# Performance work log

Measured on AMD Instinct MI355X. Metric: run time of the kernel, lower is better.

Reference implementation:

```python
import jax, jax.numpy as jnp
import numpy as np

MAX_DISP = 48


def setup_inputs() -> dict:
    key = jax.random.key(0)
    k1, k2 = jax.random.split(key)
    b, c, h, w = 2, 32, 96, 320
    left_feature = jax.random.normal(k1, (b, c, h, w), dtype=jnp.float32)
    right_feature = jax.random.normal(k2, (b, c, h, w), dtype=jnp.float32)
    return {"left_feature": left_feature, "right_feature": right_feature}


def reference(left_feature, right_feature):
    # volume[b, c, d, h, w] = left[b, c, h, w] - right[b, c, h, w - d]  if w >= d else 0
    b, c, h, w = left_feature.shape
    d_idx = jnp.arange(MAX_DISP)[:, None]          # [D, 1]
    w_idx = jnp.arange(w)[None, :]                 # [1, W]
    src = w_idx - d_idx                            # [D, W] source column in right feature
    valid = src >= 0                               # [D, W]
    src_c = jnp.clip(src, 0, w - 1)
    # gather shifted right feature: [b, c, h, D, W] -> [b, c, D, h, W]
    right_shift = right_feature[:, :, :, src_c].transpose(0, 1, 3, 2, 4)
    diff = left_feature[:, :, None, :, :] - right_shift
    volume = jnp.where(valid[None, None, :, None, :], diff, jnp.float32(0))
    return volume
```

## Files before the change

kernel.cpp:

```cpp
#include <hip/hip_runtime.h>

#define BB 2
#define CC 32
#define HH 96
#define WW 320
#define DD 48

__global__ __launch_bounds__(320) void diffvol_kernel(
        const float* __restrict__ left,
        const float* __restrict__ right,
        float* __restrict__ out) {
    __shared__ float rrow[WW];

    const int tid = threadIdx.x;
    const int blk = blockIdx.x;
    const int y   = blk % HH;
    const int bc  = blk / HH;

    const int base = (bc * HH + y) * WW;
    const float lv = left[base + tid];
    rrow[tid] = right[base + tid];
    __syncthreads();

    float* o = out + ((bc * DD) * HH + y) * WW + tid;
    const int dstride = HH * WW;

    if (tid >= 64) {
        #pragma unroll
        for (int d = 0; d < DD; ++d) {
            o[d * dstride] = lv - rrow[tid - d];
        }
    } else {
        #pragma unroll
        for (int d = 0; d < DD; ++d) {
            o[d * dstride] = (tid >= d) ? lv - rrow[tid - d] : 0.0f;
        }
    }
}

extern "C" void kernel_launch(void* const* d_in, const int* in_sizes, int n_in,
                              void* d_out, int out_size, void* d_ws, size_t ws_size,
                              hipStream_t stream) {
    const float* left  = (const float*)d_in[0];
    const float* right = (const float*)d_in[1];
    float* out = (float*)d_out;

    const int grid = BB * CC * HH;
    diffvol_kernel<<<grid, 320, 0, stream>>>(left, right, out);
}
```

Before: 388.8 us.

## Restructure grid to one block per (bc, disparity) with float4 stores and XCD-aware mapping

Each block now handles one (batch*channel, disparity) pair and walks all rows of the slice, writing contiguous float4 stores to a single output plane. Right-feature values are read directly from global memory with unaligned scalar loads, and the shared-memory staging is dropped. Block IDs are remapped so that blocks sharing a bc slice land on the same XCD for L2 reuse, and the starting row group is staggered by disparity to spread accesses. Because left and right slices are re-read once per disparity, the kernel depends on cache hits to avoid extra traffic.

```diff
diff --git a/kernel.cpp b/kernel.cpp
--- a/kernel.cpp
+++ b/kernel.cpp
@@ -5,36 +5,60 @@
 #define HH 96
 #define WW 320
 #define DD 48
+#define NBC   (BB * CC)
+#define SLICE (HH * WW)
+#define W4    (WW / 4)
+#define RPG   4
+#define NIT   (HH / RPG)
 
 __global__ __launch_bounds__(320) void diffvol_kernel(
         const float* __restrict__ left,
         const float* __restrict__ right,
         float* __restrict__ out) {
-    __shared__ float rrow[WW];
+    const int bid = blockIdx.x;
+    const int xcd = bid & 7;
+    const int loc = bid >> 3;
+    const int bc  = xcd * (NBC / 8) + loc / DD;
+    const int d   = loc % DD;
 
     const int tid = threadIdx.x;
-    const int blk = blockIdx.x;
-    const int y   = blk % HH;
-    const int bc  = blk / HH;
+    const int r   = tid / W4;
+    const int c   = tid % W4;
+    const int x0  = c * 4;
 
-    const int base = (bc * HH + y) * WW;
-    const float lv = left[base + tid];
-    rrow[tid] = right[base + tid];
-    __syncthreads();
+    const float* lslice = left  + bc * SLICE;
+    const float* rslice = right + bc * SLICE;
+    float*       oslice = out + (bc * DD + d) * SLICE;
 
-    float* o = out + ((bc * DD) * HH + y) * WW + tid;
-    const int dstride = HH * WW;
+    const int g0 = d % NIT;
+    const int sb = x0 - d;
 
-    if (tid >= 64) {
-        #pragma unroll
-        for (int d = 0; d < DD; ++d) {
-            o[d * dstride] = lv - rrow[tid - d];
+    for (int it = 0; it < NIT; ++it) {
+        int grp = it + g0; if (grp >= NIT) grp -= NIT;
+        const int y      = grp * RPG + r;
+        const int rowoff = y * WW + x0;
+
+        const float4 l4 = *reinterpret_cast<const float4*>(lslice + rowoff);
+        float4 v;
+        if (sb >= 0) {
+            const float* rp = rslice + y * WW + sb;
+            v.x = l4.x - rp[0];
+            v.y = l4.y - rp[1];
+            v.z = l4.z - rp[2];
+            v.w = l4.w - rp[3];
+        } else {
+            const float* rrow = rslice + y * WW;
+            const float lv[4] = {l4.x, l4.y, l4.z, l4.w};
+            float t[4];
+            #pragma unroll
+            for (int k = 0; k < 4; ++k) {
+                const int s = sb + k;
+                const float rv = rrow[s >= 0 ? s : 0];
+                t[k] = (s >= 0) ? lv[k] - rv : 0.0f;
+            }
+            v.x = t[0]; v.y = t[1]; v.z = t[2]; v.w = t[3];
         }
-    } else {
-        #pragma unroll
-        for (int d = 0; d < DD; ++d) {
-            o[d * dstride] = (tid >= d) ? lv - rrow[tid - d] : 0.0f;
-        }
+        *reinterpret_cast<float4*>(oslice + rowoff) = v;
     }
 }
 
@@ -45,6 +69,6 @@
     const float* right = (const float*)d_in[1];
     float* out = (float*)d_out;
 
-    const int grid = BB * CC * HH;
+    const int grid = NBC * DD;
     diffvol_kernel<<<grid, 320, 0, stream>>>(left, right, out);
 }
```

After: 415.6 us. 1.07x slower.

## Rewrite as grid-stride float4 output sweep with direct global right-row reads

Applied to the files above, without the earlier changes.

Replaces the per-row block that wrote 48 strided scalar disparity planes with a persistent grid-stride kernel. Each thread computes one contiguous float4 of the output volume, so stores are vectorized and fully sequential. Left and right values are read straight from global memory (cached) instead of through shared memory. The cost is integer division to decode indices, redundant re-reads of the input rows, and unaligned right-row loads.

```diff
diff --git a/kernel.cpp b/kernel.cpp
--- a/kernel.cpp
+++ b/kernel.cpp
@@ -5,36 +5,55 @@
 #define HH 96
 #define WW 320
 #define DD 48
+#define NBC   (BB * CC)
+#define ROWSZ WW
+#define TOT4  (BB*CC*DD*HH*WW/4)
+#define NBLK  2048
+#define NTHR  256
+#define SWEEP (NBLK * NTHR)
+#define NSW   (TOT4 / SWEEP)
 
-__global__ __launch_bounds__(320) void diffvol_kernel(
+__global__ __launch_bounds__(NTHR) void diffvol_kernel(
         const float* __restrict__ left,
         const float* __restrict__ right,
         float* __restrict__ out) {
-    __shared__ float rrow[WW];
+    const unsigned gtid = blockIdx.x * NTHR + threadIdx.x;
 
-    const int tid = threadIdx.x;
-    const int blk = blockIdx.x;
-    const int y   = blk % HH;
-    const int bc  = blk / HH;
+    #pragma unroll 1
+    for (int s = 0; s < NSW; ++s) {
+        const unsigned n   = (unsigned)s * SWEEP + gtid;
+        const unsigned x4  = n % 80;
+        const unsigned row = n / 80;
+        const unsigned bc  = row / (DD * HH);
+        const unsigned r1  = row - bc * (DD * HH);
+        const unsigned d   = r1 / HH;
+        const unsigned y   = r1 - d * HH;
+        const unsigned x0  = x4 * 4;
 
-    const int base = (bc * HH + y) * WW;
-    const float lv = left[base + tid];
-    rrow[tid] = right[base + tid];
-    __syncthreads();
+        const float* lrow = left  + (bc * HH + y) * ROWSZ;
+        const float* rrow = right + (bc * HH + y) * ROWSZ;
 
-    float* o = out + ((bc * DD) * HH + y) * WW + tid;
-    const int dstride = HH * WW;
-
-    if (tid >= 64) {
-        #pragma unroll
-        for (int d = 0; d < DD; ++d) {
-            o[d * dstride] = lv - rrow[tid - d];
+        const float4 l4 = *reinterpret_cast<const float4*>(lrow + x0);
+        const int sb = (int)x0 - (int)d;
+        float4 v;
+        if (sb >= 0) {
+            const float* rp = rrow + sb;
+            v.x = l4.x - rp[0];
+            v.y = l4.y - rp[1];
+            v.z = l4.z - rp[2];
+            v.w = l4.w - rp[3];
+        } else {
+            const float lv[4] = {l4.x, l4.y, l4.z, l4.w};
+            float t[4];
+            #pragma unroll
+            for (int k = 0; k < 4; ++k) {
+                const int src = sb + k;
+                const float rv = rrow[src >= 0 ? src : 0];
+                t[k] = (src >= 0) ? lv[k] - rv : 0.0f;
+            }
+            v = make_float4(t[0], t[1], t[2], t[3]);
         }
-    } else {
-        #pragma unroll
-        for (int d = 0; d < DD; ++d) {
-            o[d * dstride] = (tid >= d) ? lv - rrow[tid - d] : 0.0f;
-        }
+        reinterpret_cast<float4*>(out)[n] = v;
     }
 }
 
@@ -45,6 +64,5 @@
     const float* right = (const float*)d_in[1];
     float* out = (float*)d_out;
 
-    const int grid = BB * CC * HH;
-    diffvol_kernel<<<grid, 320, 0, stream>>>(left, right, out);
+    diffvol_kernel<<<NBLK, NTHR, 0, stream>>>(left, right, out);
 }
```

Result: slower. 451.1 us (+16.0%).

## Vectorize disparity volume stores as float4 and split boundary columns into separate blocks

Applied to the files above, without the earlier changes.

Each thread now produces four adjacent columns as float4 and builds the shifted right values by shuffling components of two neighbouring float4 LDS reads, so every store is 16 bytes wide. The grid is split into main blocks, which cover columns 64 and up with four rows each and need no validity check, and boundary blocks, which cover the first 64 columns with per-lane masking. The aim is to cut store instruction count and remove divergent branching in this write-bound kernel. In exchange the indexing is more complex and the two block types have uneven work.

```diff
diff --git a/kernel.cpp b/kernel.cpp
--- a/kernel.cpp
+++ b/kernel.cpp
@@ -5,35 +5,93 @@
 #define HH 96
 #define WW 320
 #define DD 48
+#define NBC    (BB*CC)
+#define W4     (WW/4)
+#define SLICE4 (HH*W4)
+#define MAIN_BLKS (NBC*24)
+#define LEFT_BLKS (NBC*6)
 
-__global__ __launch_bounds__(320) void diffvol_kernel(
+__device__ __forceinline__ float4 f4sub(float4 a, float4 b) {
+    return make_float4(a.x-b.x, a.y-b.y, a.z-b.z, a.w-b.w);
+}
+
+__global__ __launch_bounds__(256) void diffvol_kernel(
         const float* __restrict__ left,
         const float* __restrict__ right,
         float* __restrict__ out) {
-    __shared__ float rrow[WW];
+    const int bid = blockIdx.x;
+    const int tid = threadIdx.x;
 
-    const int tid = threadIdx.x;
-    const int blk = blockIdx.x;
-    const int y   = blk % HH;
-    const int bc  = blk / HH;
+    if (bid < MAIN_BLKS) {
+        __shared__ float4 rrow[4*W4];
+        const int bc = bid / 24;
+        const int y0 = (bid % 24) * 4;
+        const int r  = tid >> 6;
+        const int c4 = 16 + (tid & 63);
 
-    const int base = (bc * HH + y) * WW;
-    const float lv = left[base + tid];
-    rrow[tid] = right[base + tid];
-    __syncthreads();
+        const float4* rin = (const float4*)right + (size_t)(bc*HH + y0) * W4;
+        rrow[tid] = rin[tid];
+        if (tid < 4*W4 - 256) rrow[256 + tid] = rin[256 + tid];
+        __syncthreads();
 
-    float* o = out + ((bc * DD) * HH + y) * WW + tid;
-    const int dstride = HH * WW;
+        const float4 l4 =
+            ((const float4*)left)[(size_t)(bc*HH + y0 + r) * W4 + c4];
+        float4* o4 = (float4*)out
+                   + ((size_t)(bc*DD)*HH + (y0 + r)) * W4 + c4;
+        const float4* lds = &rrow[r * W4];
 
-    if (tid >= 64) {
+        float4 pm1 = lds[c4];
+        o4[0] = f4sub(l4, pm1);
         #pragma unroll
-        for (int d = 0; d < DD; ++d) {
-            o[d * dstride] = lv - rrow[tid - d];
+        for (int m = 1; m <= 12; ++m) {
+            const float4 pm = lds[c4 - m];
+            o4[(size_t)(4*m-3)*SLICE4] = f4sub(l4, make_float4(pm.w, pm1.x, pm1.y, pm1.z));
+            o4[(size_t)(4*m-2)*SLICE4] = f4sub(l4, make_float4(pm.z, pm.w, pm1.x, pm1.y));
+            o4[(size_t)(4*m-1)*SLICE4] = f4sub(l4, make_float4(pm.y, pm.z, pm.w, pm1.x));
+            if (m < 12)
+                o4[(size_t)(4*m)*SLICE4] = f4sub(l4, pm);
+            pm1 = pm;
         }
     } else {
+        __shared__ float4 rq[16*16];
+        const int lb = bid - MAIN_BLKS;
+        const int bc = lb / 6;
+        const int y0 = (lb % 6) * 16;
+        const int ry = tid >> 4;
+        const int c4 = tid & 15;
+        const int x0 = c4 * 4;
+
+        rq[tid] = ((const float4*)right)[(size_t)(bc*HH + y0 + ry) * W4 + c4];
+        __syncthreads();
+
+        const float4 l4 =
+            ((const float4*)left)[(size_t)(bc*HH + y0 + ry) * W4 + c4];
+        float4* o4 = (float4*)out
+                   + ((size_t)(bc*DD)*HH + (y0 + ry)) * W4 + c4;
+        const float4* lds = &rq[ry * 16];
+
+        float4 pm1 = lds[c4];
+        o4[0] = f4sub(l4, pm1);
         #pragma unroll
-        for (int d = 0; d < DD; ++d) {
-            o[d * dstride] = (tid >= d) ? lv - rrow[tid - d] : 0.0f;
+        for (int m = 1; m <= 12; ++m) {
+            const float4 pm = lds[c4 >= m ? c4 - m : 0];
+            #pragma unroll
+            for (int a = 3; a >= 0; --a) {
+                const int d = 4*m - a;
+                if (d > 47) continue;
+                float4 w;
+                if      (a == 3) w = make_float4(pm.w, pm1.x, pm1.y, pm1.z);
+                else if (a == 2) w = make_float4(pm.z, pm.w, pm1.x, pm1.y);
+                else if (a == 1) w = make_float4(pm.y, pm.z, pm.w, pm1.x);
+                else             w = pm;
+                float4 v;
+                v.x = (x0 + 0 >= d) ? l4.x - w.x : 0.0f;
+                v.y = (x0 + 1 >= d) ? l4.y - w.y : 0.0f;
+                v.z = (x0 + 2 >= d) ? l4.z - w.z : 0.0f;
+                v.w = (x0 + 3 >= d) ? l4.w - w.w : 0.0f;
+                o4[(size_t)d * SLICE4] = v;
+            }
+            pm1 = pm;
         }
     }
 }
@@ -45,6 +103,6 @@
     const float* right = (const float*)d_in[1];
     float* out = (float*)d_out;
 
-    const int grid = BB * CC * HH;
-    diffvol_kernel<<<grid, 320, 0, stream>>>(left, right, out);
+    const int grid = MAIN_BLKS + LEFT_BLKS;
+    diffvol_kernel<<<grid, 256, 0, stream>>>(left, right, out);
 }
```

After: 377.7 us. 1.03x faster.
